# Performance work log

Hardware: AMD Instinct MI355X
Metric: run time of the kernel (lower is better)

## Reference

```python
import jax, jax.numpy as jnp
import numpy as np

LPOS, LDIR, H = 10, 4, 256
N = 262144


def posenc(x, L):
    freqs = (2.0 ** jnp.arange(L)).astype(x.dtype)  # [L]
    ang = x[:, None, :] * freqs[:, None]            # [N, L, 3]
    sc = jnp.concatenate([jnp.sin(ang), jnp.cos(ang)], axis=-1)  # [N, L, 6]
    return jnp.concatenate([x, sc.reshape(x.shape[0], L * 6)], axis=1)


def _lin(key, fan_in, fan_out):
    k1, k2 = jax.random.split(key)
    bound = 1.0 / np.sqrt(fan_in)
    w = jax.random.uniform(k1, (fan_out, fan_in), jnp.float32, -bound, bound)
    b = jax.random.uniform(k2, (fan_out,), jnp.float32, -bound, bound)
    return w, b


def setup_inputs() -> dict:
    key = jax.random.key(0)
    ks = jax.random.split(key, 16)
    inp = {
        'xyz': jax.random.normal(ks[0], (N, 3), jnp.float32),
        'd': jax.random.normal(ks[1], (N, 3), jnp.float32),
    }
    in1 = LPOS * 6 + 3  # 63
    dims1 = [(in1, H), (H, H), (H, H), (H, H), (H, H)]
    for i, (fi, fo) in enumerate(dims1):
        w, b = _lin(ks[2 + i], fi, fo)
        inp[f'w1_{i}'], inp[f'b1_{i}'] = w, b
    dims2 = [(H + in1, H), (H, H), (H, H), (H, H + 1)]
    for i, (fi, fo) in enumerate(dims2):
        w, b = _lin(ks[7 + i], fi, fo)
        inp[f'w2_{i}'], inp[f'b2_{i}'] = w, b
    w, b = _lin(ks[11], H + LDIR * 6 + 3, H // 2)
    inp['wr0'], inp['br0'] = w, b
    w, b = _lin(ks[12], H // 2, 3)
    inp['wr1'], inp['br1'] = w, b
    return inp


def reference(xyz, d,
              w1_0, b1_0, w1_1, b1_1, w1_2, b1_2, w1_3, b1_3, w1_4, b1_4,
              w2_0, b2_0, w2_1, b2_1, w2_2, b2_2, w2_3, b2_3,
              wr0, br0, wr1, br1):
    relu = jax.nn.relu
    x_emb = posenc(xyz, LPOS)  # [N, 63]
    d_emb = posenc(d, LDIR)    # [N, 27]
    h = x_emb
    for w, b in ((w1_0, b1_0), (w1_1, b1_1), (w1_2, b1_2), (w1_3, b1_3), (w1_4, b1_4)):
        h = relu(h @ w.T + b)
    h = jnp.concatenate([h, x_emb], axis=1)
    for w, b in ((w2_0, b2_0), (w2_1, b2_1), (w2_2, b2_2)):
        h = relu(h @ w.T + b)
    h = h @ w2_3.T + b2_3  # [N, H+1]
    sigma = h[:, -1]
    h = h[:, :-1]
    # rgb head
    g = relu(jnp.concatenate([h, d_emb], axis=1) @ wr0.T + br0)
    c = jax.nn.sigmoid(g @ wr1.T + br1)  # [N, 3]
    return c, relu(sigma)
```

## Files before the change

### kernel.cpp

```cpp
#include <hip/hip_runtime.h>

#define NPTS 262144
#define SA 328
#define SB 264
#define LDS_BYTES ((128*SA + 128*SB)*2)

typedef __attribute__((ext_vector_type(8))) short short8;
typedef __attribute__((ext_vector_type(4))) float f32x4;

__device__ __forceinline__ ushort bfu(float f) {
  union { float f; unsigned u; } x; x.f = f;
  unsigned r = x.u + 0x7fffu + ((x.u >> 16) & 1u);
  return (ushort)(r >> 16);
}

__global__ void pack_w(const float* __restrict__ w, ushort* __restrict__ dst,
                       int OUT, int KIN, int nct, int nkt) {
  int t = blockIdx.x * 256 + threadIdx.x;
  int total = nct * nkt * 64;
  if (t >= total) return;
  int l  = t & 63;
  int kt = (t >> 6) % nkt;
  int ct = (t >> 6) / nkt;
  int row = ct * 16 + (l & 15);
  int k0  = kt * 32 + (l >> 4) * 8;
  ushort* d = dst + (size_t)t * 8;
  #pragma unroll
  for (int j = 0; j < 8; ++j) {
    int k = k0 + j;
    float v = (row < OUT && k < KIN) ? w[(size_t)row * KIN + k] : 0.f;
    d[j] = bfu(v);
  }
}

__global__ void pack_b(const float* __restrict__ b, float* __restrict__ dst, int OUT, int OUTP) {
  int i = blockIdx.x * 256 + threadIdx.x;
  if (i < OUTP) dst[i] = (i < OUT) ? b[i] : 0.f;
}

template<int NKT, int KSPLIT, int NC, bool RELU>
__device__ __forceinline__ void layerg(
    const ushort* __restrict__ wpk, const float* __restrict__ bias,
    const ushort* a0, int s0, const ushort* a1, int s1,
    ushort* dst, int sd, int dstCol0,
    int mbase, int ctBase, int lane)
{
  const int lr = lane & 15, lk = lane >> 4;
  f32x4 acc[4][NC];
  #pragma unroll
  for (int c = 0; c < NC; ++c) {
    float b = bias[(ctBase + c) * 16 + lr];
    #pragma unroll
    for (int r = 0; r < 4; ++r) acc[r][c] = (f32x4){b, b, b, b};
  }
  #pragma unroll 2
  for (int kt = 0; kt < NKT; ++kt) {
    short8 av[4];
    if (kt < KSPLIT) {
      int ko = kt * 32 + lk * 8;
      #pragma unroll
      for (int r = 0; r < 4; ++r)
        av[r] = *(const short8*)(a0 + (size_t)(mbase + r * 16 + lr) * s0 + ko);
    } else {
      int ko = (kt - KSPLIT) * 32 + lk * 8;
      #pragma unroll
      for (int r = 0; r < 4; ++r)
        av[r] = *(const short8*)(a1 + (size_t)(mbase + r * 16 + lr) * s1 + ko);
    }
    #pragma unroll
    for (int c = 0; c < NC; ++c) {
      short8 bv = *(const short8*)(wpk + (size_t)(((ctBase + c) * NKT + kt) * 64 + lane) * 8);
      #pragma unroll
      for (int r = 0; r < 4; ++r)
        acc[r][c] = __builtin_amdgcn_mfma_f32_16x16x32_bf16(av[r], bv, acc[r][c], 0, 0, 0);
    }
  }
  #pragma unroll
  for (int c = 0; c < NC; ++c)
    #pragma unroll
    for (int r = 0; r < 4; ++r)
      #pragma unroll
      for (int i = 0; i < 4; ++i) {
        float v = acc[r][c][i];
        if (RELU) v = fmaxf(v, 0.f);
        dst[(size_t)(mbase + r * 16 + lk * 4 + i) * sd + dstCol0 + (ctBase + c) * 16 + lr] = bfu(v);
      }
}

extern __shared__ ushort smem[];

__global__ __launch_bounds__(512, 2) void nerf_fused(
    const float* __restrict__ xyz, const float* __restrict__ dvec,
    const ushort* __restrict__ wp, const float* __restrict__ bp,
    float* __restrict__ out)
{
  ushort* bufA = smem;
  ushort* bufB = smem + 128 * SA;
  const int tid  = threadIdx.x;
  const int row0 = blockIdx.x * 128;
  const int wave = tid >> 6, lane = tid & 63;
  const int mw = wave >> 2, cg = wave & 3;
  const int mbase = mw * 64;
  const int lr = lane & 15, lk = lane >> 4;

  {
    int r = tid >> 2, j = tid & 3;
    const float* x = xyz + (size_t)(row0 + r) * 3;
    float x0 = x[0], x1 = x[1], x2 = x[2];
    ushort* dst = bufA + (size_t)r * SA + 256;
    if (j == 3) { dst[0] = bfu(x0); dst[1] = bfu(x1); dst[2] = bfu(x2); dst[63] = 0; }
    for (int l = j; l < 10; l += 4) {
      float f = (float)(1 << l);
      int b = 3 + l * 6;
      dst[b + 0] = bfu(__sinf(x0 * f)); dst[b + 1] = bfu(__sinf(x1 * f)); dst[b + 2] = bfu(__sinf(x2 * f));
      dst[b + 3] = bfu(__cosf(x0 * f)); dst[b + 4] = bfu(__cosf(x1 * f)); dst[b + 5] = bfu(__cosf(x2 * f));
    }
  }
  __syncthreads();
  layerg<2, 2, 4, true >(wp + 0,      bp + 0,    bufA + 256, SA, bufA, SA, bufB, SB, 0, mbase, cg * 4, lane);
  __syncthreads();
  layerg<8, 8, 4, true >(wp + 16384,  bp + 256,  bufB, SB, bufB, SB, bufA, SA, 0, mbase, cg * 4, lane);
  __syncthreads();
  layerg<8, 8, 4, true >(wp + 81920,  bp + 512,  bufA, SA, bufA, SA, bufB, SB, 0, mbase, cg * 4, lane);
  __syncthreads();
  layerg<8, 8, 4, true >(wp + 147456, bp + 768,  bufB, SB, bufB, SB, bufA, SA, 0, mbase, cg * 4, lane);
  __syncthreads();
  layerg<8, 8, 4, true >(wp + 212992, bp + 1024, bufA, SA, bufA, SA, bufB, SB, 0, mbase, cg * 4, lane);
  __syncthreads();
  layerg<10, 8, 4, true>(wp + 278528, bp + 1280, bufB, SB, bufA + 256, SA, bufA, SA, 0, mbase, cg * 4, lane);
  __syncthreads();
  layerg<8, 8, 4, true >(wp + 360448, bp + 1536, bufA, SA, bufA, SA, bufB, SB, 0, mbase, cg * 4, lane);
  __syncthreads();
  layerg<8, 8, 4, true >(wp + 425984, bp + 1792, bufB, SB, bufB, SB, bufA, SA, 0, mbase, cg * 4, lane);
  __syncthreads();
  layerg<8, 8, 4, false>(wp + 491520, bp + 2048, bufA, SA, bufA, SA, bufB, SB, 0, mbase, cg * 4, lane);
  if (cg == 0) {
    const ushort* w23 = wp + 491520;
    float bb = bp[2048 + 256 + lr];
    f32x4 acc2[4];
    #pragma unroll
    for (int r = 0; r < 4; ++r) acc2[r] = (f32x4){bb, bb, bb, bb};
    #pragma unroll 2
    for (int kt = 0; kt < 8; ++kt) {
      short8 bv = *(const short8*)(w23 + (size_t)((16 * 8 + kt) * 64 + lane) * 8);
      #pragma unroll
      for (int r = 0; r < 4; ++r) {
        short8 av = *(const short8*)(bufA + (size_t)(mbase + r * 16 + lr) * SA + kt * 32 + lk * 8);
        acc2[r] = __builtin_amdgcn_mfma_f32_16x16x32_bf16(av, bv, acc2[r], 0, 0, 0);
      }
    }
    if (lr == 0) {
      #pragma unroll
      for (int r = 0; r < 4; ++r)
        #pragma unroll
        for (int i = 0; i < 4; ++i)
          out[(size_t)3 * NPTS + row0 + mbase + r * 16 + lk * 4 + i] = fmaxf(acc2[r][i], 0.f);
    }
  }
  __syncthreads();
  {
    int r = tid >> 2, j = tid & 3;
    const float* x = dvec + (size_t)(row0 + r) * 3;
    float x0 = x[0], x1 = x[1], x2 = x[2];
    ushort* dst = bufA + (size_t)r * SA;
    if (j == 3) {
      dst[0] = bfu(x0); dst[1] = bfu(x1); dst[2] = bfu(x2);
      #pragma unroll
      for (int q = 27; q < 32; ++q) dst[q] = 0;
    }
    {
      int l = j;
      float f = (float)(1 << l);
      int b = 3 + l * 6;
      dst[b + 0] = bfu(__sinf(x0 * f)); dst[b + 1] = bfu(__sinf(x1 * f)); dst[b + 2] = bfu(__sinf(x2 * f));
      dst[b + 3] = bfu(__cosf(x0 * f)); dst[b + 4] = bfu(__cosf(x1 * f)); dst[b + 5] = bfu(__cosf(x2 * f));
    }
  }
  __syncthreads();
  layerg<9, 8, 2, true>(wp + 561152, bp + 2320, bufB, SB, bufA, SA, bufA, SA, 128, mbase, cg * 2, lane);
  __syncthreads();
  {
    const ushort* w = wp + 598016;
    float bb = bp[2448 + lr];
    f32x4 acc = (f32x4){bb, bb, bb, bb};
    #pragma unroll
    for (int kt = 0; kt < 4; ++kt) {
      short8 av = *(const short8*)(bufA + (size_t)(wave * 16 + lr) * SA + 128 + kt * 32 + lk * 8);
      short8 bv = *(const short8*)(w + (size_t)(kt * 64 + lane) * 8);
      acc = __builtin_amdgcn_mfma_f32_16x16x32_bf16(av, bv, acc, 0, 0, 0);
    }
    if (lr < 3) {
      #pragma unroll
      for (int i = 0; i < 4; ++i) {
        int grow = row0 + wave * 16 + lk * 4 + i;
        out[(size_t)grow * 3 + lr] = 1.f / (1.f + __expf(-acc[i]));
      }
    }
  }
}

extern "C" void kernel_launch(void* const* d_in, const int* in_sizes, int n_in,
                              void* d_out, int out_size, void* d_ws, size_t ws_size,
                              hipStream_t stream) {
  const float* xyz  = (const float*)d_in[0];
  const float* dvec = (const float*)d_in[1];
  ushort* wp = (ushort*)d_ws;
  float*  bp = (float*)((char*)d_ws + 1200128);

  struct WSpec { int idx, OUT, KIN, nct, nkt, off; };
  const WSpec wspecs[11] = {
    { 2, 256,  63, 16,  2,      0},
    { 4, 256, 256, 16,  8,  16384},
    { 6, 256, 256, 16,  8,  81920},
    { 8, 256, 256, 16,  8, 147456},
    {10, 256, 256, 16,  8, 212992},
    {12, 256, 319, 16, 10, 278528},
    {14, 256, 256, 16,  8, 360448},
    {16, 256, 256, 16,  8, 425984},
    {18, 257, 256, 17,  8, 491520},
    {20, 128, 283,  8,  9, 561152},
    {22,   3, 128,  1,  4, 598016},
  };
  for (int i = 0; i < 11; ++i) {
    int total = wspecs[i].nct * wspecs[i].nkt * 64;
    pack_w<<<dim3((total + 255) / 256), dim3(256), 0, stream>>>(
      (const float*)d_in[wspecs[i].idx], wp + wspecs[i].off,
      wspecs[i].OUT, wspecs[i].KIN, wspecs[i].nct, wspecs[i].nkt);
  }
  struct BSpec { int idx, OUT, OUTP, off; };
  const BSpec bspecs[11] = {
    { 3, 256, 256,    0}, { 5, 256, 256,  256}, { 7, 256, 256,  512}, { 9, 256, 256,  768},
    {11, 256, 256, 1024}, {13, 256, 256, 1280}, {15, 256, 256, 1536}, {17, 256, 256, 1792},
    {19, 257, 272, 2048}, {21, 128, 128, 2320}, {23,   3,  16, 2448},
  };
  for (int i = 0; i < 11; ++i) {
    pack_b<<<dim3((bspecs[i].OUTP + 255) / 256), dim3(256), 0, stream>>>(
      (const float*)d_in[bspecs[i].idx], bp + bspecs[i].off, bspecs[i].OUT, bspecs[i].OUTP);
  }

  hipFuncSetAttribute(reinterpret_cast<const void*>(nerf_fused),
                      hipFuncAttributeMaxDynamicSharedMemorySize, LDS_BYTES);
  nerf_fused<<<dim3(2048), dim3(512), LDS_BYTES, stream>>>(xyz, dvec, wp, bp, (float*)d_out);
}
```

Before: 404.6 us.

## Halve rows per block, swap MFMA operands for packed bf16 stores

Reduces the per-block row tile from 128 to 64, so each of the 8 waves owns all 64 rows and 2 column tiles instead of splitting rows between two wave groups. This halves LDS per block and raises the launch-bounds occupancy target to 4 blocks per CU. The MFMA operands are swapped so the accumulator is transposed, which lets each lane write 4 consecutive bf16 outputs as one packed 8-byte LDS store and load the bias as a vector. The trade-off is that each wave now reloads weight fragments for fewer output columns per activation load, increasing weight traffic per row, with added register-pressure risk from the 4-block target.

```diff
diff --git a/kernel.cpp b/kernel.cpp
--- a/kernel.cpp
+++ b/kernel.cpp
@@ -1,9 +1,11 @@
 #include <hip/hip_runtime.h>
+#include <hip/hip_bf16.h>
 
 #define NPTS 262144
+#define ROWS 64
 #define SA 328
 #define SB 264
-#define LDS_BYTES ((128*SA + 128*SB)*2)
+#define LDS_BYTES ((ROWS*SA + ROWS*SB)*2)
 
 typedef __attribute__((ext_vector_type(8))) short short8;
 typedef __attribute__((ext_vector_type(4))) float f32x4;
@@ -12,6 +14,11 @@
   union { float f; unsigned u; } x; x.f = f;
   unsigned r = x.u + 0x7fffu + ((x.u >> 16) & 1u);
   return (ushort)(r >> 16);
+}
+
+__device__ __forceinline__ unsigned pk2(float a, float b) {
+  __hip_bfloat162 h = __float22bfloat162_rn(float2{a, b});
+  return *reinterpret_cast<unsigned*>(&h);
 }
 
 __global__ void pack_w(const float* __restrict__ w, ushort* __restrict__ dst,
@@ -43,73 +50,73 @@
     const ushort* __restrict__ wpk, const float* __restrict__ bias,
     const ushort* a0, int s0, const ushort* a1, int s1,
     ushort* dst, int sd, int dstCol0,
-    int mbase, int ctBase, int lane)
+    int ctBase, int lane)
 {
   const int lr = lane & 15, lk = lane >> 4;
   f32x4 acc[4][NC];
   #pragma unroll
   for (int c = 0; c < NC; ++c) {
-    float b = bias[(ctBase + c) * 16 + lr];
-    #pragma unroll
-    for (int r = 0; r < 4; ++r) acc[r][c] = (f32x4){b, b, b, b};
-  }
-  #pragma unroll 2
+    f32x4 b4 = *(const f32x4*)(bias + (ctBase + c) * 16 + lk * 4);
+    #pragma unroll
+    for (int r = 0; r < 4; ++r) acc[r][c] = b4;
+  }
+  #pragma unroll 4
   for (int kt = 0; kt < NKT; ++kt) {
     short8 av[4];
     if (kt < KSPLIT) {
       int ko = kt * 32 + lk * 8;
       #pragma unroll
       for (int r = 0; r < 4; ++r)
-        av[r] = *(const short8*)(a0 + (size_t)(mbase + r * 16 + lr) * s0 + ko);
+        av[r] = *(const short8*)(a0 + (size_t)(r * 16 + lr) * s0 + ko);
     } else {
       int ko = (kt - KSPLIT) * 32 + lk * 8;
       #pragma unroll
       for (int r = 0; r < 4; ++r)
-        av[r] = *(const short8*)(a1 + (size_t)(mbase + r * 16 + lr) * s1 + ko);
+        av[r] = *(const short8*)(a1 + (size_t)(r * 16 + lr) * s1 + ko);
     }
     #pragma unroll
     for (int c = 0; c < NC; ++c) {
       short8 bv = *(const short8*)(wpk + (size_t)(((ctBase + c) * NKT + kt) * 64 + lane) * 8);
       #pragma unroll
       for (int r = 0; r < 4; ++r)
-        acc[r][c] = __builtin_amdgcn_mfma_f32_16x16x32_bf16(av[r], bv, acc[r][c], 0, 0, 0);
+        acc[r][c] = __builtin_amdgcn_mfma_f32_16x16x32_bf16(bv, av[r], acc[r][c], 0, 0, 0);
     }
   }
   #pragma unroll
   for (int c = 0; c < NC; ++c)
     #pragma unroll
-    for (int r = 0; r < 4; ++r)
-      #pragma unroll
-      for (int i = 0; i < 4; ++i) {
-        float v = acc[r][c][i];
-        if (RELU) v = fmaxf(v, 0.f);
-        dst[(size_t)(mbase + r * 16 + lk * 4 + i) * sd + dstCol0 + (ctBase + c) * 16 + lr] = bfu(v);
+    for (int r = 0; r < 4; ++r) {
+      float v0 = acc[r][c][0], v1 = acc[r][c][1], v2 = acc[r][c][2], v3 = acc[r][c][3];
+      if (RELU) {
+        v0 = fmaxf(v0, 0.f); v1 = fmaxf(v1, 0.f);
+        v2 = fmaxf(v2, 0.f); v3 = fmaxf(v3, 0.f);
       }
+      uint2 p; p.x = pk2(v0, v1); p.y = pk2(v2, v3);
+      *(uint2*)(dst + (size_t)(r * 16 + lr) * sd + dstCol0 + (ctBase + c) * 16 + lk * 4) = p;
+    }
 }
 
 extern __shared__ ushort smem[];
 
-__global__ __launch_bounds__(512, 2) void nerf_fused(
+__global__ __launch_bounds__(512, 4) void nerf_fused(
     const float* __restrict__ xyz, const float* __restrict__ dvec,
     const ushort* __restrict__ wp, const float* __restrict__ bp,
     float* __restrict__ out)
 {
   ushort* bufA = smem;
-  ushort* bufB = smem + 128 * SA;
+  ushort* bufB = smem + ROWS * SA;
   const int tid  = threadIdx.x;
-  const int row0 = blockIdx.x * 128;
+  const int row0 = blockIdx.x * ROWS;
   const int wave = tid >> 6, lane = tid & 63;
-  const int mw = wave >> 2, cg = wave & 3;
-  const int mbase = mw * 64;
   const int lr = lane & 15, lk = lane >> 4;
 
   {
-    int r = tid >> 2, j = tid & 3;
+    int r = tid >> 3, j = tid & 7;
     const float* x = xyz + (size_t)(row0 + r) * 3;
     float x0 = x[0], x1 = x[1], x2 = x[2];
     ushort* dst = bufA + (size_t)r * SA + 256;
-    if (j == 3) { dst[0] = bfu(x0); dst[1] = bfu(x1); dst[2] = bfu(x2); dst[63] = 0; }
-    for (int l = j; l < 10; l += 4) {
+    if (j == 7) { dst[0] = bfu(x0); dst[1] = bfu(x1); dst[2] = bfu(x2); dst[63] = 0; }
+    for (int l = j; l < 10; l += 8) {
       float f = (float)(1 << l);
       int b = 3 + l * 6;
       dst[b + 0] = bfu(__sinf(x0 * f)); dst[b + 1] = bfu(__sinf(x1 * f)); dst[b + 2] = bfu(__sinf(x2 * f));
@@ -117,24 +124,24 @@
     }
   }
   __syncthreads();
-  layerg<2, 2, 4, true >(wp + 0,      bp + 0,    bufA + 256, SA, bufA, SA, bufB, SB, 0, mbase, cg * 4, lane);
-  __syncthreads();
-  layerg<8, 8, 4, true >(wp + 16384,  bp + 256,  bufB, SB, bufB, SB, bufA, SA, 0, mbase, cg * 4, lane);
-  __syncthreads();
-  layerg<8, 8, 4, true >(wp + 81920,  bp + 512,  bufA, SA, bufA, SA, bufB, SB, 0, mbase, cg * 4, lane);
-  __syncthreads();
-  layerg<8, 8, 4, true >(wp + 147456, bp + 768,  bufB, SB, bufB, SB, bufA, SA, 0, mbase, cg * 4, lane);
-  __syncthreads();
-  layerg<8, 8, 4, true >(wp + 212992, bp + 1024, bufA, SA, bufA, SA, bufB, SB, 0, mbase, cg * 4, lane);
-  __syncthreads();
-  layerg<10, 8, 4, true>(wp + 278528, bp + 1280, bufB, SB, bufA + 256, SA, bufA, SA, 0, mbase, cg * 4, lane);
-  __syncthreads();
-  layerg<8, 8, 4, true >(wp + 360448, bp + 1536, bufA, SA, bufA, SA, bufB, SB, 0, mbase, cg * 4, lane);
-  __syncthreads();
-  layerg<8, 8, 4, true >(wp + 425984, bp + 1792, bufB, SB, bufB, SB, bufA, SA, 0, mbase, cg * 4, lane);
-  __syncthreads();
-  layerg<8, 8, 4, false>(wp + 491520, bp + 2048, bufA, SA, bufA, SA, bufB, SB, 0, mbase, cg * 4, lane);
-  if (cg == 0) {
+  layerg<2, 2, 2, true >(wp + 0,      bp + 0,    bufA + 256, SA, bufA, SA, bufB, SB, 0, wave * 2, lane);
+  __syncthreads();
+  layerg<8, 8, 2, true >(wp + 16384,  bp + 256,  bufB, SB, bufB, SB, bufA, SA, 0, wave * 2, lane);
+  __syncthreads();
+  layerg<8, 8, 2, true >(wp + 81920,  bp + 512,  bufA, SA, bufA, SA, bufB, SB, 0, wave * 2, lane);
+  __syncthreads();
+  layerg<8, 8, 2, true >(wp + 147456, bp + 768,  bufB, SB, bufB, SB, bufA, SA, 0, wave * 2, lane);
+  __syncthreads();
+  layerg<8, 8, 2, true >(wp + 212992, bp + 1024, bufA, SA, bufA, SA, bufB, SB, 0, wave * 2, lane);
+  __syncthreads();
+  layerg<10, 8, 2, true>(wp + 278528, bp + 1280, bufB, SB, bufA + 256, SA, bufA, SA, 0, wave * 2, lane);
+  __syncthreads();
+  layerg<8, 8, 2, true >(wp + 360448, bp + 1536, bufA, SA, bufA, SA, bufB, SB, 0, wave * 2, lane);
+  __syncthreads();
+  layerg<8, 8, 2, true >(wp + 425984, bp + 1792, bufB, SB, bufB, SB, bufA, SA, 0, wave * 2, lane);
+  __syncthreads();
+  layerg<8, 8, 2, false>(wp + 491520, bp + 2048, bufA, SA, bufA, SA, bufB, SB, 0, wave * 2, lane);
+  if (wave == 0) {
     const ushort* w23 = wp + 491520;
     float bb = bp[2048 + 256 + lr];
     f32x4 acc2[4];
@@ -145,7 +152,7 @@
       short8 bv = *(const short8*)(w23 + (size_t)((16 * 8 + kt) * 64 + lane) * 8);
       #pragma unroll
       for (int r = 0; r < 4; ++r) {
-        short8 av = *(const short8*)(bufA + (size_t)(mbase + r * 16 + lr) * SA + kt * 32 + lk * 8);
+        short8 av = *(const short8*)(bufA + (size_t)(r * 16 + lr) * SA + kt * 32 + lk * 8);
         acc2[r] = __builtin_amdgcn_mfma_f32_16x16x32_bf16(av, bv, acc2[r], 0, 0, 0);
       }
     }
@@ -154,32 +161,31 @@
       for (int r = 0; r < 4; ++r)
         #pragma unroll
         for (int i = 0; i < 4; ++i)
-          out[(size_t)3 * NPTS + row0 + mbase + r * 16 + lk * 4 + i] = fmaxf(acc2[r][i], 0.f);
+          out[(size_t)3 * NPTS + row0 + r * 16 + lk * 4 + i] = fmaxf(acc2[r][i], 0.f);
     }
   }
   __syncthreads();
   {
-    int r = tid >> 2, j = tid & 3;
+    int r = tid >> 3, j = tid & 7;
     const float* x = dvec + (size_t)(row0 + r) * 3;
     float x0 = x[0], x1 = x[1], x2 = x[2];
     ushort* dst = bufA + (size_t)r * SA;
-    if (j == 3) {
+    if (j == 7) {
       dst[0] = bfu(x0); dst[1] = bfu(x1); dst[2] = bfu(x2);
       #pragma unroll
       for (int q = 27; q < 32; ++q) dst[q] = 0;
     }
-    {
-      int l = j;
-      float f = (float)(1 << l);
-      int b = 3 + l * 6;
+    if (j < 4) {
+      float f = (float)(1 << j);
+      int b = 3 + j * 6;
       dst[b + 0] = bfu(__sinf(x0 * f)); dst[b + 1] = bfu(__sinf(x1 * f)); dst[b + 2] = bfu(__sinf(x2 * f));
       dst[b + 3] = bfu(__cosf(x0 * f)); dst[b + 4] = bfu(__cosf(x1 * f)); dst[b + 5] = bfu(__cosf(x2 * f));
     }
   }
   __syncthreads();
-  layerg<9, 8, 2, true>(wp + 561152, bp + 2320, bufB, SB, bufA, SA, bufA, SA, 128, mbase, cg * 2, lane);
-  __syncthreads();
-  {
+  layerg<9, 8, 1, true>(wp + 561152, bp + 2320, bufB, SB, bufA, SA, bufA, SA, 128, wave, lane);
+  __syncthreads();
+  if (wave < 4) {
     const ushort* w = wp + 598016;
     float bb = bp[2448 + lr];
     f32x4 acc = (f32x4){bb, bb, bb, bb};
@@ -240,5 +246,5 @@
 
   hipFuncSetAttribute(reinterpret_cast<const void*>(nerf_fused),
                       hipFuncAttributeMaxDynamicSharedMemorySize, LDS_BYTES);
-  nerf_fused<<<dim3(2048), dim3(512), LDS_BYTES, stream>>>(xyz, dvec, wp, bp, (float*)d_out);
-}
+  nerf_fused<<<dim3(NPTS / ROWS), dim3(512), LDS_BYTES, stream>>>(xyz, dvec, wp, bp, (float*)d_out);
+}
```

Result: faster. 370.3 us (-8.5%).
